# Optimization experiments

Hardware: AMD Instinct MI355X
Metric: run time of the kernel (lower is better)

The kernel has to match this reference:

```python
import jax, jax.numpy as jnp
import numpy as np
import math

SQRT2 = math.sqrt(2.0)


def _rotation_grids(theta_deg, grid_size):
    # torch affine_grid (align_corners=True) base coords for output [G, G]:
    # grid[h, w] = (xs[w], ys[h]) transformed by R = [[c, s, 0], [-s, c, 0]]
    xs = jnp.linspace(-1.0, 1.0, grid_size, dtype=jnp.float32)
    X, Y = jnp.meshgrid(xs, xs)            # [G,G], X varies along width
    th = jnp.deg2rad(theta_deg.astype(jnp.float32))[:, None, None]  # [T,1,1]
    c, s = jnp.cos(th), jnp.sin(th)
    gx = c * X + s * Y                      # [T,G,G]
    gy = -s * X + c * Y
    return gx, gy


def _bilinear_sample(x, gx, gy):
    # x: [N,C,H,W]; gx,gy: [T,G,G] normalized coords in [-1,1]
    # bilinear, zeros padding, align_corners=True -> returns [N,C,T,G,G]
    N, C, H, W = x.shape
    ix = (gx + 1.0) * 0.5 * (W - 1)
    iy = (gy + 1.0) * 0.5 * (H - 1)
    ix0 = jnp.floor(ix)
    iy0 = jnp.floor(iy)
    wx1 = ix - ix0
    wy1 = iy - iy0
    wx0 = 1.0 - wx1
    wy0 = 1.0 - wy1

    def gather(iyf, ixf):
        valid = (ixf >= 0) & (ixf <= W - 1) & (iyf >= 0) & (iyf <= H - 1)
        ii = jnp.clip(ixf, 0, W - 1).astype(jnp.int32)
        jj = jnp.clip(iyf, 0, H - 1).astype(jnp.int32)
        v = x[:, :, jj, ii]                 # [N,C,T,G,G]
        return v * valid.astype(x.dtype)

    return (gather(iy0, ix0) * (wy0 * wx0)
            + gather(iy0, ix0 + 1) * (wy0 * wx1)
            + gather(iy0 + 1, ix0) * (wy1 * wx0)
            + gather(iy0 + 1, ix0 + 1) * (wy1 * wx1))


def radon_forward(x, theta_deg):
    N, C, W, H = x.shape
    # circle=False: pad image to the diagonal size so rotations keep all content
    diagonal = SQRT2 * W
    pad = int(math.ceil(diagonal - W))
    new_center = (W + pad) // 2
    old_center = W // 2
    pad_before = new_center - old_center
    x = jnp.pad(x, ((0, 0), (0, 0), (pad_before, pad - pad_before),
                    (pad_before, pad - pad_before)))
    G = x.shape[-1]                         # padded grid size == ceil(sqrt2*W)
    gx, gy = _rotation_grids(theta_deg, G)  # [T,G,G]
    rotated = _bilinear_sample(x, gx, gy)   # [N,C,T,G,G]
    sino = rotated.sum(axis=3)              # integrate over rows -> [N,C,T,G]
    return jnp.swapaxes(sino, 2, 3)         # [N,C,G,T]


def setup_inputs() -> dict:
    key = jax.random.key(0)
    x = jax.random.normal(key, (2, 1, 256, 256), dtype=jnp.float32)
    theta = jnp.arange(180, dtype=jnp.int64) if jax.config.jax_enable_x64 else jnp.arange(180, dtype=jnp.int32)
    return {"x": x, "theta": theta}


def reference(x, theta):
    return radon_forward(x, theta)
```

## Files before the change

### kernel.cpp

```cpp
#include <hip/hip_runtime.h>
#include <hip/hip_fp16.h>
#include <math.h>


#define G       363
#define NT      180
#define PADB    53
#define STEP    (2.0f / 362.0f)
#define DEG2RAD 0.017453292519943295f

#define TSW     32
#define NJB     12
#define NJBF    6
#define CW      264
#define CH      264
#define NWSLOT  (NT * NJB * 2 * 2)
#define NTUPLE  (NWSLOT * 8)

#define GLOAD16(gp, lp) __builtin_amdgcn_global_load_lds(                     \
    (const __attribute__((address_space(1))) void*)(gp),                      \
    (__attribute__((address_space(3))) void*)(lp), 16, 0, 0)

__global__ __launch_bounds__(256) void radon_fwd(
    const float* __restrict__ x, const int* __restrict__ theta,
    float* __restrict__ out)
{
    const int t = blockIdx.x / NJBF, jb = blockIdx.x % NJBF;
    const int jl = threadIdx.x, chunk = threadIdx.y;
    const int j = jb * 64 + jl;
    const float th = (float)theta[t] * DEG2RAD;
    const float c = cosf(th), s = sinf(th);
    const float xj = fmaf((float)j, STEP, -1.0f);
    const float s181 = s * 181.0f, c181 = c * 181.0f;
    const float bx = fmaf(c, xj, 1.0f) * 181.0f;
    const float by = fmaf(-s, xj, 1.0f) * 181.0f;
    const float* img0 = x;
    const float* img1 = x + 65536;
    float acc0 = 0.f, acc1 = 0.f;
    for (int i = chunk; i < G; i += 4) {
        const float xi = fmaf((float)i, STEP, -1.0f);
        const float ix = fmaf(s181, xi, bx);
        const float iy = fmaf(c181, xi, by);
        const float fx = floorf(ix), fy = floorf(iy);
        const int ix0 = (int)fx, iy0 = (int)fy;
        const float wx1 = ix - fx, wy1 = iy - fy;
        const float wx0 = 1.f - wx1, wy0 = 1.f - wy1;
        const int cc0 = ix0 - 53, cc1 = cc0 + 1, rr0 = iy0 - 53, rr1 = rr0 + 1;
        const float wxa = ((unsigned)cc0 < 256u) ? wx0 : 0.f;
        const float wxb = ((unsigned)cc1 < 256u) ? wx1 : 0.f;
        const float wya = ((unsigned)rr0 < 256u) ? wy0 : 0.f;
        const float wyb = ((unsigned)rr1 < 256u) ? wy1 : 0.f;
        const int c0c = min(max(cc0, 0), 255), c1c = min(max(cc1, 0), 255);
        const int r0b = min(max(rr0, 0), 255) << 8, r1b = min(max(rr1, 0), 255) << 8;
        const float w00 = wya * wxa, w01 = wya * wxb, w10 = wyb * wxa, w11 = wyb * wxb;
        acc0 = fmaf(img0[r0b + c0c], w00, acc0);
        acc0 = fmaf(img0[r0b + c1c], w01, acc0);
        acc0 = fmaf(img0[r1b + c0c], w10, acc0);
        acc0 = fmaf(img0[r1b + c1c], w11, acc0);
        acc1 = fmaf(img1[r0b + c0c], w00, acc1);
        acc1 = fmaf(img1[r0b + c1c], w01, acc1);
        acc1 = fmaf(img1[r1b + c0c], w10, acc1);
        acc1 = fmaf(img1[r1b + c1c], w11, acc1);
    }
    __shared__ float red[2][4][64];
    red[0][chunk][jl] = acc0;
    red[1][chunk][jl] = acc1;
    __syncthreads();
    if (threadIdx.y < 2 && j < G) {
        const int n = threadIdx.y;
        out[n * (G * NT) + j * NT + t] =
            red[n][0][jl] + red[n][1][jl] + red[n][2][jl] + red[n][3][jl];
    }
}

__global__ __launch_bounds__(256) void prep_k(
    const float* __restrict__ x, const int* __restrict__ theta,
    unsigned* __restrict__ xIh, unsigned* __restrict__ xTIh,
    int2* __restrict__ bbox)
{
    const int bid = blockIdx.x;
    const int tx = threadIdx.x, ty = threadIdx.y;
    const int tid = ty * 32 + tx;

    if (bid < 81) {
        __shared__ unsigned tl[32][33];
        const int cx0 = (bid % 9) * 32, cy0 = (bid / 9) * 32;
        #pragma unroll
        for (int dy = 0; dy < 32; dy += 8) {
            const int cy = cy0 + ty + dy, cx = cx0 + tx;
            const int pr = cy - 4, pc = cx - 4;
            unsigned v = 0u;
            if ((unsigned)pr < 256u && (unsigned)pc < 256u) {
                const int p = pr * 256 + pc;
                const unsigned short a = __half_as_ushort(__float2half_rn(x[p]));
                const unsigned short b = __half_as_ushort(__float2half_rn(x[p + 65536]));
                v = (unsigned)a | ((unsigned)b << 16);
            }
            if (cy < CH && cx < CW) xIh[cy * CW + cx] = v;
            tl[ty + dy][tx] = v;
        }
        __syncthreads();
        #pragma unroll
        for (int dy = 0; dy < 32; dy += 8) {
            const int rp = cx0 + ty + dy, cp = cy0 + tx;
            if (rp < CH && cp < CW) xTIh[rp * CW + cp] = tl[tx][ty + dy];
        }
    } else {
        const int tuple = (bid - 81) * 256 + tid;
        if (tuple < NTUPLE) {
            const int sub = tuple & 7;
            const int ws  = tuple >> 3;
            const int wi  = ws & 1;
            const int wj  = (ws >> 1) & 1;
            const int jb  = (ws >> 2) % NJB;
            const int t   = (ws >> 2) / NJB;

            const float th = (float)theta[t] * DEG2RAD;
            const float c = cosf(th), s = sinf(th);
            const float s181 = s * 181.0f, c181 = c * 181.0f;
            const int caseA = (fabsf(c) >= fabsf(s));
            const float slopeU = caseA ? c181 : s181;
            const float slopeV = caseA ? s181 : c181;
            const float dU = slopeU * STEP;
            const float dV = slopeV * STEP;

            const int   j0  = jb * 32 + wj * 16;
            const float xjm = fmaf((float)j0,        STEP, -1.0f);
            const float xjM = fmaf((float)(j0 + 15), STEP, -1.0f);
            const float bxm = fmaf(c,  xjm, 1.0f) * 181.0f;
            const float bym = fmaf(-s, xjm, 1.0f) * 181.0f;
            const float bxM = fmaf(c,  xjM, 1.0f) * 181.0f;
            const float byM = fmaf(-s, xjM, 1.0f) * 181.0f;
            const float U00m = (caseA ? bym : bxm) - slopeU;
            const float U00M = (caseA ? byM : bxM) - slopeU;
            const float V00m = (caseA ? bxm : bym) - slopeV;
            const float V00M = (caseA ? bxM : byM) - slopeV;

            const int i0 = (wi * 8 + sub) * 24;
            const float fi0 = (float)i0, fi1 = (float)(i0 + 23);
            const float Umin = fminf(fminf(fmaf(dU, fi0, U00m), fmaf(dU, fi0, U00M)),
                                     fminf(fmaf(dU, fi1, U00m), fmaf(dU, fi1, U00M)));
            const float Vmin = fminf(fminf(fmaf(dV, fi0, V00m), fmaf(dV, fi0, V00M)),
                                     fminf(fmaf(dV, fi1, V00m), fmaf(dV, fi1, V00M)));
            const int r0 = (int)floorf(Umin) - 1;
            const int c0 = (int)floorf(Vmin) - 1;
            bbox[tuple] = make_int2(r0, c0);
        }
    }
}

template<bool SAFE>
__device__ __forceinline__ void stage32(char* tileW_b,
    const unsigned* __restrict__ srcC, int r0p, int c0p, int lane)
{
    const int ty0 = lane >> 3;
    const int tx  = (lane & 7) << 2;
    #pragma unroll
    for (int u = 0; u < 4; ++u) {
        const int ty = ty0 + (u << 3);
        int idx;
        if (SAFE) {
            idx = (r0p + 4 + ty) * CW + (c0p + 4 + tx);
        } else {
            const int rc = min(max(r0p + ty, -4), 256) + 4;
            const int cc = min(max(c0p + tx, -4), 256) + 4;
            idx = rc * CW + cc;
        }
        GLOAD16(srcC + idx, tileW_b + (u << 10));
    }
}

template<bool TAIL>
__device__ __forceinline__ void gather6(const unsigned* __restrict__ tl,
    float Uf0, float Vf0, float dU, float dV, int iexc,
    float& a0, float& a1)
{
    __half2 acc = __float2half2_rn(0.0f);
    #pragma unroll
    for (int k = 0; k < 6; ++k) {
        const float Uf = fmaf((float)k, dU, Uf0);
        const float Vf = fmaf((float)k, dV, Vf0);
        const float fU = floorf(Uf), fV = floorf(Vf);
        const float wU1 = Uf - fU;
        const float wV1 = Vf - fV;
        const int rel = (int)fmaf(fU, (float)TSW, fV);
        const __half2 x00 = *(const __half2*)(tl + rel);
        const __half2 x01 = *(const __half2*)(tl + rel + 1);
        const __half2 x10 = *(const __half2*)(tl + rel + TSW);
        const __half2 x11 = *(const __half2*)(tl + rel + TSW + 1);
        const __half2 wv2 = __float2half2_rn(wV1);
        const __half2 wu2 = __float2half2_rn(wU1);
        const __half2 t0 = __hfma2(wv2, __hsub2(x01, x00), x00);
        const __half2 t1 = __hfma2(wv2, __hsub2(x11, x10), x10);
        __half2 v = __hfma2(wu2, __hsub2(t1, t0), t0);
        if (TAIL && k >= iexc) v = __float2half2_rn(0.0f);
        acc = __hadd2(acc, v);
    }
    a0 += __low2float(acc);
    a1 += __high2float(acc);
}

__global__ __launch_bounds__(256) void radon_wv5(
    const unsigned* __restrict__ xIh, const unsigned* __restrict__ xTIh,
    const int* __restrict__ theta, const int4* __restrict__ bbox4,
    float* __restrict__ out)
{
    __shared__ unsigned tile[4 * TSW * TSW];
    __shared__ float red[4][2][16];

    const int blk  = blockIdx.x;
    const int t    = blk / NJB;
    const int jb   = blk - t * NJB;
    const int tid  = threadIdx.x;
    const int lane = tid & 63;
    const int wid  = tid >> 6;
    const int wj   = wid & 1;
    const int wi   = wid >> 1;
    const int jl   = lane & 15;
    const int kk   = lane >> 4;

    unsigned* tileW = tile + wid * (TSW * TSW);
    char*     tileW_b = (char*)tileW;

    const int ws = ((t * NJB + jb) * 2 + wj) * 2 + wi;
    const int4 bb0 = bbox4[ws * 4 + 0];
    const int4 bb1 = bbox4[ws * 4 + 1];
    const int4 bb2 = bbox4[ws * 4 + 2];
    const int4 bb3 = bbox4[ws * 4 + 3];

    const float th = (float)theta[t] * DEG2RAD;
    const float c = cosf(th), s = sinf(th);
    const float s181 = s * 181.0f, c181 = c * 181.0f;

    const int caseA = (fabsf(c) >= fabsf(s));
    const unsigned* __restrict__ srcC = caseA ? xIh : xTIh;

    const float slopeU = caseA ? c181 : s181;
    const float slopeV = caseA ? s181 : c181;
    const float dU = slopeU * STEP;
    const float dV = slopeV * STEP;

    const int   j  = jb * 32 + wj * 16 + jl;
    const float xj = fmaf((float)j, STEP, -1.0f);
    const float bx = fmaf(c,  xj, 1.0f) * 181.0f;
    const float by = fmaf(-s, xj, 1.0f) * 181.0f;
    const float U00L = (caseA ? by : bx) - slopeU;
    const float V00L = (caseA ? bx : by) - slopeV;

    const float fiofs = (float)(kk * 6);

    float a0 = 0.f, a1 = 0.f;

    #pragma unroll
    for (int sub = 0; sub < 8; ++sub) {
        int r0i, c0i;
        if      (sub == 0) { r0i = bb0.x; c0i = bb0.y; }
        else if (sub == 1) { r0i = bb0.z; c0i = bb0.w; }
        else if (sub == 2) { r0i = bb1.x; c0i = bb1.y; }
        else if (sub == 3) { r0i = bb1.z; c0i = bb1.w; }
        else if (sub == 4) { r0i = bb2.x; c0i = bb2.y; }
        else if (sub == 5) { r0i = bb2.z; c0i = bb2.w; }
        else if (sub == 6) { r0i = bb3.x; c0i = bb3.y; }
        else               { r0i = bb3.z; c0i = bb3.w; }
        const int r0 = __builtin_amdgcn_readfirstlane(r0i);
        const int c0 = __builtin_amdgcn_readfirstlane(c0i);
        const int r0p = r0 - PADB, c0p = c0 - PADB;

        asm volatile("s_waitcnt lgkmcnt(0)" ::: "memory");
        __builtin_amdgcn_sched_barrier(0);

        if (r0p >= -4 && r0p <= 228 && c0p >= -4 && c0p <= 228)
            stage32<true >(tileW_b, srcC, r0p, c0p, lane);
        else
            stage32<false>(tileW_b, srcC, r0p, c0p, lane);

        asm volatile("s_waitcnt vmcnt(0)" ::: "memory");
        __builtin_amdgcn_sched_barrier(0);

        const int i0 = (wi * 8 + sub) * 24;
        const float fi  = (float)i0 + fiofs;
        const float Uf0 = fmaf(dU, fi, U00L) - (float)r0;
        const float Vf0 = fmaf(dV, fi, V00L) - (float)c0;
        const int ibase = i0 + kk * 6;

        if (i0 + 23 < G) {
            gather6<false>(tileW, Uf0, Vf0, dU, dV, 6, a0, a1);
        } else {
            gather6<true>(tileW, Uf0, Vf0, dU, dV, G - ibase, a0, a1);
        }
    }

    a0 += __shfl_xor(a0, 16); a1 += __shfl_xor(a1, 16);
    a0 += __shfl_xor(a0, 32); a1 += __shfl_xor(a1, 32);

    if (lane < 16) {
        red[wid][0][lane] = a0;
        red[wid][1][lane] = a1;
    }
    __syncthreads();

    if (tid < 64) {
        const int n = tid >> 5, jj = tid & 31;
        const int wj2 = jj >> 4, jl2 = jj & 15;
        const float v = red[wj2][n][jl2] + red[wj2 + 2][n][jl2];
        const int jo = jb * 32 + jj;
        if (jo < G)
            out[(n * G + jo) * NT + t] = v;
    }
}

extern "C" void kernel_launch(void* const* d_in, const int* in_sizes, int n_in,
                              void* d_out, int out_size, void* d_ws, size_t ws_size,
                              hipStream_t stream) {
    const float* x     = (const float*)d_in[0];
    const int*   theta = (const int*)d_in[1];
    float*       out   = (float*)d_out;

    const size_t XIH_OFF  = 0;
    const size_t XTIH_OFF = (size_t)CH * CW * 4;
    const size_t BBOX_OFF = 2 * XTIH_OFF;
    const size_t NEED     = BBOX_OFF + (size_t)NTUPLE * 8;

    if (ws_size < NEED) {
        hipLaunchKernelGGL(radon_fwd, dim3(NT * NJBF), dim3(64, 4), 0, stream,
                           x, theta, out);
        return;
    }

    unsigned* xIh  = (unsigned*)((char*)d_ws + XIH_OFF);
    unsigned* xTIh = (unsigned*)((char*)d_ws + XTIH_OFF);
    int2*     bbox = (int2*)((char*)d_ws + BBOX_OFF);

    hipLaunchKernelGGL(prep_k, dim3(351), dim3(32, 8), 0, stream,
                       x, theta, xIh, xTIh, bbox);
    hipLaunchKernelGGL(radon_wv5, dim3(NT * NJB), dim3(256), 0, stream,
                       xIh, xTIh, theta, (const int4*)bbox, out);
}
```

Before: 32.04 us.

## Double-buffer per-wave LDS tiles to overlap next tile load with gather

Each wave now owns two 32x32 LDS tile buffers. It issues the global_load_lds for sub-tile sub+1 before gathering from sub-tile sub, waiting only on the older loads with vmcnt(4). This hides global load latency behind the bilinear gather math. LDS use per block doubles to 32KB, which may lower occupancy, and the reduction scratch now reuses the tile buffers.

```diff
diff --git a/kernel.cpp b/kernel.cpp
--- a/kernel.cpp
+++ b/kernel.cpp
@@ -150,7 +150,7 @@
 }
 
 template<bool SAFE>
-__device__ __forceinline__ void stage32(char* tileW_b,
+__device__ __forceinline__ void stage32(char* buf_b,
     const unsigned* __restrict__ srcC, int r0p, int c0p, int lane)
 {
     const int ty0 = lane >> 3;
@@ -166,7 +166,7 @@
             const int cc = min(max(c0p + tx, -4), 256) + 4;
             idx = rc * CW + cc;
         }
-        GLOAD16(srcC + idx, tileW_b + (u << 10));
+        GLOAD16(srcC + idx, buf_b + (u << 10));
     }
 }
 
@@ -200,13 +200,12 @@
     a1 += __high2float(acc);
 }
 
-__global__ __launch_bounds__(256) void radon_wv5(
+__global__ __launch_bounds__(256) void radon_wv6(
     const unsigned* __restrict__ xIh, const unsigned* __restrict__ xTIh,
     const int* __restrict__ theta, const int4* __restrict__ bbox4,
     float* __restrict__ out)
 {
-    __shared__ unsigned tile[4 * TSW * TSW];
-    __shared__ float red[4][2][16];
+    __shared__ unsigned tile[4 * 2 * TSW * TSW];
 
     const int blk  = blockIdx.x;
     const int t    = blk / NJB;
@@ -219,8 +218,7 @@
     const int jl   = lane & 15;
     const int kk   = lane >> 4;
 
-    unsigned* tileW = tile + wid * (TSW * TSW);
-    char*     tileW_b = (char*)tileW;
+    unsigned* tileW = tile + wid * (2 * TSW * TSW);
 
     const int ws = ((t * NJB + jb) * 2 + wj) * 2 + wi;
     const int4 bb0 = bbox4[ws * 4 + 0];
@@ -251,58 +249,79 @@
 
     float a0 = 0.f, a1 = 0.f;
 
+    auto origin = [&](int u, int& r, int& cc) {
+        if      (u == 0) { r = bb0.x; cc = bb0.y; }
+        else if (u == 1) { r = bb0.z; cc = bb0.w; }
+        else if (u == 2) { r = bb1.x; cc = bb1.y; }
+        else if (u == 3) { r = bb1.z; cc = bb1.w; }
+        else if (u == 4) { r = bb2.x; cc = bb2.y; }
+        else if (u == 5) { r = bb2.z; cc = bb2.w; }
+        else if (u == 6) { r = bb3.x; cc = bb3.y; }
+        else             { r = bb3.z; cc = bb3.w; }
+    };
+    auto dostage = [&](int bufsel, int r0, int c0) {
+        char* b = (char*)(tileW + bufsel * (TSW * TSW));
+        const int r0p = r0 - PADB, c0p = c0 - PADB;
+        if (r0p >= -4 && r0p <= 228 && c0p >= -4 && c0p <= 228)
+            stage32<true >(b, srcC, r0p, c0p, lane);
+        else
+            stage32<false>(b, srcC, r0p, c0p, lane);
+    };
+
+    int r0i, c0i;
+    origin(0, r0i, c0i);
+    int r0c = __builtin_amdgcn_readfirstlane(r0i);
+    int c0c = __builtin_amdgcn_readfirstlane(c0i);
+    dostage(0, r0c, c0c);
+
     #pragma unroll
     for (int sub = 0; sub < 8; ++sub) {
-        int r0i, c0i;
-        if      (sub == 0) { r0i = bb0.x; c0i = bb0.y; }
-        else if (sub == 1) { r0i = bb0.z; c0i = bb0.w; }
-        else if (sub == 2) { r0i = bb1.x; c0i = bb1.y; }
-        else if (sub == 3) { r0i = bb1.z; c0i = bb1.w; }
-        else if (sub == 4) { r0i = bb2.x; c0i = bb2.y; }
-        else if (sub == 5) { r0i = bb2.z; c0i = bb2.w; }
-        else if (sub == 6) { r0i = bb3.x; c0i = bb3.y; }
-        else               { r0i = bb3.z; c0i = bb3.w; }
-        const int r0 = __builtin_amdgcn_readfirstlane(r0i);
-        const int c0 = __builtin_amdgcn_readfirstlane(c0i);
-        const int r0p = r0 - PADB, c0p = c0 - PADB;
-
-        asm volatile("s_waitcnt lgkmcnt(0)" ::: "memory");
+        int r0n = 0, c0n = 0;
+        if (sub < 7) {
+            origin(sub + 1, r0i, c0i);
+            r0n = __builtin_amdgcn_readfirstlane(r0i);
+            c0n = __builtin_amdgcn_readfirstlane(c0i);
+            asm volatile("s_waitcnt lgkmcnt(0)" ::: "memory");
+            __builtin_amdgcn_sched_barrier(0);
+            dostage((sub + 1) & 1, r0n, c0n);
+            asm volatile("s_waitcnt vmcnt(4)" ::: "memory");
+        } else {
+            asm volatile("s_waitcnt vmcnt(0)" ::: "memory");
+        }
         __builtin_amdgcn_sched_barrier(0);
 
-        if (r0p >= -4 && r0p <= 228 && c0p >= -4 && c0p <= 228)
-            stage32<true >(tileW_b, srcC, r0p, c0p, lane);
-        else
-            stage32<false>(tileW_b, srcC, r0p, c0p, lane);
-
-        asm volatile("s_waitcnt vmcnt(0)" ::: "memory");
-        __builtin_amdgcn_sched_barrier(0);
-
+        const unsigned* buf = tileW + (sub & 1) * (TSW * TSW);
         const int i0 = (wi * 8 + sub) * 24;
         const float fi  = (float)i0 + fiofs;
-        const float Uf0 = fmaf(dU, fi, U00L) - (float)r0;
-        const float Vf0 = fmaf(dV, fi, V00L) - (float)c0;
+        const float Uf0 = fmaf(dU, fi, U00L) - (float)r0c;
+        const float Vf0 = fmaf(dV, fi, V00L) - (float)c0c;
         const int ibase = i0 + kk * 6;
 
         if (i0 + 23 < G) {
-            gather6<false>(tileW, Uf0, Vf0, dU, dV, 6, a0, a1);
+            gather6<false>(buf, Uf0, Vf0, dU, dV, 6, a0, a1);
         } else {
-            gather6<true>(tileW, Uf0, Vf0, dU, dV, G - ibase, a0, a1);
-        }
+            gather6<true>(buf, Uf0, Vf0, dU, dV, G - ibase, a0, a1);
+        }
+
+        r0c = r0n; c0c = c0n;
     }
 
     a0 += __shfl_xor(a0, 16); a1 += __shfl_xor(a1, 16);
     a0 += __shfl_xor(a0, 32); a1 += __shfl_xor(a1, 32);
 
+    float* redw = (float*)tileW;
     if (lane < 16) {
-        red[wid][0][lane] = a0;
-        red[wid][1][lane] = a1;
+        redw[lane]      = a0;
+        redw[16 + lane] = a1;
     }
     __syncthreads();
 
     if (tid < 64) {
         const int n = tid >> 5, jj = tid & 31;
         const int wj2 = jj >> 4, jl2 = jj & 15;
-        const float v = red[wj2][n][jl2] + red[wj2 + 2][n][jl2];
+        const float* rA = (const float*)(tile + wj2       * (2 * TSW * TSW));
+        const float* rB = (const float*)(tile + (wj2 + 2) * (2 * TSW * TSW));
+        const float v = rA[n * 16 + jl2] + rB[n * 16 + jl2];
         const int jo = jb * 32 + jj;
         if (jo < G)
             out[(n * G + jo) * NT + t] = v;
@@ -333,6 +352,6 @@
 
     hipLaunchKernelGGL(prep_k, dim3(351), dim3(32, 8), 0, stream,
                        x, theta, xIh, xTIh, bbox);
-    hipLaunchKernelGGL(radon_wv5, dim3(NT * NJB), dim3(256), 0, stream,
+    hipLaunchKernelGGL(radon_wv6, dim3(NT * NJB), dim3(256), 0, stream,
                        xIh, xTIh, theta, (const int4*)bbox, out);
 }
```

Measured after the change: 33.20 us. 1.04x slower.
